# Optimization experiments

Measured on AMD Instinct MI355X. Metric: run time of the kernel, lower is better.

Reference implementation:

```python
import jax, jax.numpy as jnp
import numpy as np

# dims matching init_kwargs
B = 4096
NFIELD = 20
NFEAT = 100000
SQL_NEMB = 16
DATA_NEMB = 16
HID = 512
K = 16          # num_experts
C = 2           # select_experts (top-k)
OUT = 1
CARD = NFIELD + NFEAT + 1  # sql embedding rows
GATE_IN = NFIELD * SQL_NEMB   # 320
EXP_IN = NFIELD * DATA_NEMB   # 320
EPS = 1e-10


def _xavier(key, shape):
    fan_in, fan_out = shape[-2], shape[-1]
    a = np.sqrt(6.0 / (fan_in + fan_out)).astype(np.float32)
    return jax.random.uniform(key, shape, jnp.float32, -a, a)


def setup_inputs() -> dict:
    key = jax.random.key(0)
    ks = jax.random.split(key, 12)
    x = jax.random.randint(ks[0], (B, NFIELD), 0, NFEAT, dtype=jnp.int64)
    sql = jax.random.randint(ks[1], (B, NFIELD), 0, CARD, dtype=jnp.int64)
    return {
        "x": x,
        "sql": sql,
        "sql_emb_w": _xavier(ks[2], (CARD, SQL_NEMB)),
        "inp_emb_w": _xavier(ks[3], (NFEAT, DATA_NEMB)),
        # gate network: Linear(GATE_IN->HID) + relu + Linear(HID->K) + softmax
        "gw1": _xavier(ks[4], (GATE_IN, HID)),
        "gb1": jnp.zeros((HID,), jnp.float32),
        "gw2": _xavier(ks[5], (HID, K)),
        "gb2": jnp.zeros((K,), jnp.float32),
        # K expert DNNs: Linear(EXP_IN->HID) + relu + Linear(HID->OUT)
        "ew1": _xavier(ks[6], (K, EXP_IN, HID)),
        "eb1": jnp.zeros((K, HID), jnp.float32),
        "ew2": _xavier(ks[7], (K, HID, OUT)),
        "eb2": jnp.zeros((K, OUT), jnp.float32),
    }


def _cv_squared(v):
    # coefficient-of-variation squared, Shazeer-style load-balancing term
    return jnp.var(v) / (jnp.mean(v) ** 2 + EPS)


def reference(x, sql, sql_emb_w, inp_emb_w, gw1, gb1, gw2, gb2, ew1, eb1, ew2, eb2):
    b = x.shape[0]
    x_emb = inp_emb_w[x].reshape(b, -1)      # [B, NFIELD*DATA_NEMB]
    sql_emb = sql_emb_w[sql].reshape(b, -1)  # [B, NFIELD*SQL_NEMB]

    # gate network -> softmax scores over K experts
    h = jax.nn.relu(sql_emb @ gw1 + gb1)
    gate_scores = jax.nn.softmax(h @ gw2 + gb2, axis=-1)  # [B, K]

    # top-C sparse gating: keep top-C scores, renormalize, zero the rest
    top_v, top_i = jax.lax.top_k(gate_scores, C)
    top_v = top_v / jnp.sum(top_v, axis=-1, keepdims=True)
    gates = jnp.zeros((b, K), gate_scores.dtype).at[jnp.arange(b)[:, None], top_i].set(top_v)

    # expert MLPs (batched over expert dim; zero gates nullify unselected experts)
    eh = jax.nn.relu(jnp.einsum('bi,kih->bkh', x_emb, ew1) + eb1)   # [B, K, HID]
    eo = jnp.einsum('bkh,kho->bko', eh, ew2) + eb2                   # [B, K, OUT]
    y = jnp.sum(gates[:, :, None] * eo, axis=1).squeeze(-1)          # [B]

    importance = jnp.sum(gates, axis=0)                              # [K]
    load = jnp.sum((gates > 0).astype(gates.dtype), axis=0)         # [K]
    loss = _cv_squared(importance) + _cv_squared(load)
    return y, loss
```

## Files before the change

kernel.cpp:

```cpp
#include <hip/hip_runtime.h>

#define Bn 4096
#define NF 20
#define NEMB 16
#define HIDN 512
#define KE 16
#define GIN 320
#define NKS 10

typedef __attribute__((ext_vector_type(8))) short short8;
typedef __attribute__((ext_vector_type(4))) float f32x4;

__device__ __forceinline__ unsigned short f2bf(float f) {
  unsigned int u = __builtin_bit_cast(unsigned int, f);
  u += 0x7fff + ((u >> 16) & 1);
  return (unsigned short)(u >> 16);
}
__device__ __forceinline__ float bf2f(unsigned short h) {
  unsigned int u = ((unsigned int)h) << 16;
  return __builtin_bit_cast(float, u);
}

__device__ __forceinline__ void gload_lds16(const unsigned short* g, void* l) {
  __builtin_amdgcn_global_load_lds(
      (const __attribute__((address_space(1))) unsigned int*)g,
      (__attribute__((address_space(3))) unsigned int*)l, 16, 0, 0);
}

__device__ __forceinline__ void vwait(int n) {
  if (n >= 5) asm volatile("s_waitcnt vmcnt(5)" ::: "memory");
  else        asm volatile("s_waitcnt vmcnt(0)" ::: "memory");
  __builtin_amdgcn_sched_barrier(0);
}

__global__ __launch_bounds__(256) void prep_kernel(
    const int* __restrict__ sql, const float* __restrict__ semb,
    const float* __restrict__ gw1, const float* __restrict__ ew1,
    unsigned short* __restrict__ SH, unsigned short* __restrict__ SL,
    unsigned short* __restrict__ GWF, unsigned short* __restrict__ EWF,
    float* __restrict__ y, int* __restrict__ cnt) {
  long long t = (long long)blockIdx.x * 256 + threadIdx.x;
  if (t < 81920) {
    int row = (int)(t / NF), f = (int)(t % NF);
    int idx = sql[row * NF + f];
    const float4* s = (const float4*)(semb + (size_t)idx * NEMB);
    float4 v[4] = {s[0], s[1], s[2], s[3]};
    const float* sf = (const float*)v;
    short8 h0, h1, l0, l1;
#pragma unroll
    for (int i = 0; i < 8; i++) {
      float a = sf[i];
      unsigned short hb = f2bf(a);
      h0[i] = (short)hb; l0[i] = (short)f2bf(a - bf2f(hb));
      a = sf[8 + i];
      hb = f2bf(a);
      h1[i] = (short)hb; l1[i] = (short)f2bf(a - bf2f(hb));
    }
    size_t o = (size_t)row * GIN + f * NEMB;
    *(short8*)(SH + o) = h0; *(short8*)(SH + o + 8) = h1;
    *(short8*)(SL + o) = l0; *(short8*)(SL + o + 8) = l1;
    return;
  }
  t -= 81920;
  if (t < 40960) {
    int s = (int)(t / 20480), r = (int)(t % 20480);
    int ks = r / 2048, r2 = r % 2048, nt = r2 / 64, l = r2 % 64;
    int k0 = ks * 32 + (l >> 4) * 8, n = nt * 16 + (l & 15);
    short8 o;
#pragma unroll
    for (int j = 0; j < 8; j++) {
      float w = gw1[(size_t)(k0 + j) * HIDN + n];
      unsigned short hb = f2bf(w);
      o[j] = (s == 0) ? (short)hb : (short)f2bf(w - bf2f(hb));
    }
    *(short8*)(GWF + ((((size_t)s * NKS + ks) * 32 + nt) * 64 + l) * 8) = o;
    return;
  }
  t -= 40960;
  if (t < 327680) {
    int e = (int)(t / 20480), r = (int)(t % 20480);
    int ks = r / 2048, r2 = r % 2048, nt = r2 / 64, l = r2 % 64;
    int k0 = ks * 32 + (l >> 4) * 8, n = nt * 16 + (l & 15);
    const float* W = ew1 + (size_t)e * GIN * HIDN;
    short8 o;
#pragma unroll
    for (int j = 0; j < 8; j++) o[j] = (short)f2bf(W[(size_t)(k0 + j) * HIDN + n]);
    *(short8*)(EWF + ((((size_t)e * NKS + ks) * 32 + nt) * 64 + l) * 8) = o;
    return;
  }
  t -= 327680;
  if (t < Bn + 1) y[t] = 0.f;
  else if (t < Bn + 1 + KE) cnt[t - (Bn + 1)] = 0;
}

__global__ __launch_bounds__(256, 2) void gate_kernel(
    const unsigned short* __restrict__ SH, const unsigned short* __restrict__ SL,
    const unsigned short* __restrict__ GWF, const float* __restrict__ gb1,
    const float* __restrict__ gw2, float* __restrict__ glp) {
  __shared__ __align__(16) unsigned short ring[3][10240];
  __shared__ float hs[64][68];
  const int tid = threadIdx.x, lane = tid & 63, wv = tid >> 6;
  const int band = blockIdx.x * 64, cb = blockIdx.y;
  const int ntg = cb * 4 + wv;

  short8 bh[NKS], bl[NKS];
#pragma unroll
  for (int ks = 0; ks < NKS; ks++) {
    bh[ks] = *(const short8*)(GWF + ((size_t)(ks * 32 + ntg)) * 512 + lane * 8);
    bl[ks] = *(const short8*)(GWF + ((size_t)((NKS + ks) * 32 + ntg)) * 512 + lane * 8);
  }
  const int cl = wv * 16 + (lane & 15);
  const float b1v = gb1[cb * 64 + cl];
  __builtin_amdgcn_sched_barrier(0);

#define GSTG(pi, slot)                                                        \
  {                                                                           \
    _Pragma("unroll") for (int i = 0; i < 5; i++) {                           \
      int c = wv * 5 + i;                                                     \
      int hl = c >= 10, kss = c - hl * 10;                                    \
      const unsigned short* s_ = (hl ? SL : SH) +                             \
          (size_t)(band + (pi) * 16 + (lane & 15)) * GIN + kss * 32 +         \
          (lane >> 4) * 8;                                                    \
      gload_lds16(s_, &ring[slot][c * 512 + lane * 8]);                       \
    }                                                                         \
  }

  GSTG(0, 0) GSTG(1, 1)
  __builtin_amdgcn_sched_barrier(0);

#pragma unroll
  for (int p = 0; p < 4; p++) {
    vwait(p < 3 ? 5 : 0);
    __builtin_amdgcn_s_barrier();
    __builtin_amdgcn_sched_barrier(0);
    if (p + 2 < 4) GSTG(p + 2, (p + 2) % 3)
    __builtin_amdgcn_sched_barrier(0);
    const unsigned short* rb = ring[p % 3];
    f32x4 acc = {};
#pragma unroll
    for (int ks = 0; ks < NKS; ks++) {
      short8 ah = *(const short8*)&rb[ks * 512 + lane * 8];
      short8 al = *(const short8*)&rb[(NKS + ks) * 512 + lane * 8];
      acc = __builtin_amdgcn_mfma_f32_16x16x32_bf16(ah, bh[ks], acc, 0, 0, 0);
      acc = __builtin_amdgcn_mfma_f32_16x16x32_bf16(al, bh[ks], acc, 0, 0, 0);
      acc = __builtin_amdgcn_mfma_f32_16x16x32_bf16(ah, bl[ks], acc, 0, 0, 0);
    }
#pragma unroll
    for (int j = 0; j < 4; j++)
      hs[p * 16 + (lane >> 4) * 4 + j][cl] = fmaxf(acc[j] + b1v, 0.f);
  }
  __syncthreads();

  float (*g2s)[16] = (float(*)[16])&ring[0][0];
  ((float4*)g2s)[tid] = ((const float4*)(gw2 + (size_t)cb * 64 * KE))[tid];
  __syncthreads();
#pragma unroll
  for (int it = 0; it < 4; it++) {
    int row = it * 16 + (tid >> 4), q = tid & 15;
    float s = 0.f;
#pragma unroll 8
    for (int c = 0; c < 64; c++) s = fmaf(hs[row][c], g2s[c][q], s);
    glp[((size_t)cb * Bn + band + row) * KE + q] = s;
  }
#undef GSTG
}

__global__ __launch_bounds__(256) void gate2_kernel(
    const float* __restrict__ glp, const float* __restrict__ gb2,
    int* __restrict__ cnt, int* __restrict__ list, float* __restrict__ wlist) {
  __shared__ int lcnt[KE];
  __shared__ int gbase[KE];
  const int tid = threadIdx.x;
  const int row = blockIdx.x * 256 + tid;
  if (tid < KE) lcnt[tid] = 0;
  __syncthreads();
  float lg[KE];
  {
    const float4* c = (const float4*)gb2;
#pragma unroll
    for (int u = 0; u < 4; u++) {
      float4 s = c[u];
      lg[u * 4 + 0] = s.x; lg[u * 4 + 1] = s.y;
      lg[u * 4 + 2] = s.z; lg[u * 4 + 3] = s.w;
    }
#pragma unroll
    for (int sl = 0; sl < 8; sl++) {
      const float4* a = (const float4*)(glp + ((size_t)sl * Bn + row) * KE);
#pragma unroll
      for (int u = 0; u < 4; u++) {
        float4 v = a[u];
        lg[u * 4 + 0] += v.x; lg[u * 4 + 1] += v.y;
        lg[u * 4 + 2] += v.z; lg[u * 4 + 3] += v.w;
      }
    }
  }
  float m = lg[0];
#pragma unroll
  for (int q = 1; q < KE; q++) m = fmaxf(m, lg[q]);
  float e[KE];
#pragma unroll
  for (int q = 0; q < KE; q++) e[q] = expf(lg[q] - m);
  int i1 = 0; float v1 = e[0];
#pragma unroll
  for (int q = 1; q < KE; q++) if (e[q] > v1) { v1 = e[q]; i1 = q; }
  int i2 = (i1 == 0) ? 1 : 0; float v2 = e[i2];
#pragma unroll
  for (int q = 0; q < KE; q++)
    if (q != i1 && e[q] > v2) { v2 = e[q]; i2 = q; }
  int o1 = atomicAdd(&lcnt[i1], 1);
  int o2 = atomicAdd(&lcnt[i2], 1);
  __syncthreads();
  if (tid < KE) gbase[tid] = atomicAdd(&cnt[tid], lcnt[tid]);
  __syncthreads();
  float den = v1 + v2;
  int s1 = gbase[i1] + o1;
  list[i1 * Bn + s1] = row; wlist[i1 * Bn + s1] = v1 / den;
  int s2 = gbase[i2] + o2;
  list[i2 * Bn + s2] = row; wlist[i2 * Bn + s2] = v2 / den;
}

__global__ __launch_bounds__(256) void packloss_kernel(
    const int* __restrict__ x, const float* __restrict__ demb,
    const int* __restrict__ cnt, const int* __restrict__ list,
    const float* __restrict__ wlist, unsigned short* __restrict__ XEP,
    float* __restrict__ out) {
  __shared__ float simp[KE][KE];
  __shared__ float fimp[KE];
  const int tid = threadIdx.x;
  const int jb = blockIdx.x, k = blockIdx.y;
  if (jb == 64) {
    if (k != 0) return;
    const int kk = tid >> 4, g = tid & 15;
    const int n = cnt[kk];
    float s = 0.f;
    for (int j = g; j < n; j += 16) s += wlist[kk * Bn + j];
    simp[kk][g] = s;
    __syncthreads();
    if (tid < KE) {
      float t = 0.f;
      for (int q = 0; q < KE; q++) t += simp[tid][q];
      fimp[tid] = t;
    }
    __syncthreads();
    if (tid == 0) {
      double mi = 0.0, ml = 0.0;
      for (int q = 0; q < KE; q++) { mi += fimp[q]; ml += (double)cnt[q]; }
      mi /= KE; ml /= KE;
      double vi = 0.0, vl = 0.0;
      for (int q = 0; q < KE; q++) {
        double di = fimp[q] - mi; vi += di * di;
        double dl = (double)cnt[q] - ml; vl += dl * dl;
      }
      vi /= KE; vl /= KE;
      out[Bn] = (float)(vi / (mi * mi + 1e-10) + vl / (ml * ml + 1e-10));
    }
    return;
  }
  const int n = cnt[k];
  if (jb * 64 >= n) return;
  unsigned short* reg = XEP + (size_t)k * 1310720;
#pragma unroll
  for (int it = 0; it < 5; it++) {
    int tt = it * 256 + tid;
    int i = jb * 64 + tt / NF, f = tt % NF;
    if (i < n) {
      int rid = list[k * Bn + i];
      int idx = x[rid * NF + f];
      const float4* s = (const float4*)(demb + (size_t)idx * NEMB);
      float4 v[4] = {s[0], s[1], s[2], s[3]};
      const float* sf = (const float*)v;
      short8 o0, o1;
#pragma unroll
      for (int e = 0; e < 8; e++) {
        o0[e] = (short)f2bf(sf[e]);
        o1[e] = (short)f2bf(sf[8 + e]);
      }
      int panel = i >> 5, mt = (i >> 4) & 1, lr = i & 15;
      int ks = f >> 1, ko0 = (f & 1) * 2;
      unsigned short* d =
          reg + (size_t)panel * 10240 + ks * 1024 + mt * 512 + ko0 * 128 + lr * 8;
      *(short8*)d = o0;
      *(short8*)(d + 128) = o1;
    }
  }
}

__global__ __launch_bounds__(256, 2) void expert_kernel(
    const unsigned short* __restrict__ XEP, const unsigned short* __restrict__ EWF,
    const float* __restrict__ eb1, const float* __restrict__ ew2,
    const float* __restrict__ eb2, const int* __restrict__ cnt,
    const int* __restrict__ list, const float* __restrict__ wlist,
    float* __restrict__ y) {
  __shared__ __align__(16) unsigned short ring[3][10240];
  __shared__ float pb[16][4][32];
  const int tid = threadIdx.x, lane = tid & 63, wv = tid >> 6;
  const int cb = blockIdx.x, k = blockIdx.y, qz = blockIdx.z;
  const int n = cnt[k];
  const int np = (n + 31) >> 5;
  const int npb = (np > qz) ? ((np - qz + 7) >> 3) : 0;
  if (npb == 0) return;
  const unsigned short* XEPk = XEP + (size_t)k * 1310720;
  const int kBn = k * Bn;

  float b1v[2], w2v[2];
#pragma unroll
  for (int nt = 0; nt < 2; nt++) {
    int colg = cb * 128 + (wv * 2 + nt) * 16 + (lane & 15);
    b1v[nt] = eb1[(size_t)k * HIDN + colg];
    w2v[nt] = ew2[(size_t)k * HIDN + colg];
  }
  short8 bb[2][NKS];
#pragma unroll
  for (int nt = 0; nt < 2; nt++)
#pragma unroll
    for (int ks = 0; ks < NKS; ks++)
      bb[nt][ks] = *(const short8*)(
          EWF + ((size_t)((k * NKS + ks) * 32 + cb * 8 + wv * 2 + nt)) * 512 +
          lane * 8);
  __builtin_amdgcn_sched_barrier(0);

#define ESTG(pi, slot)                                                        \
  {                                                                           \
    _Pragma("unroll") for (int i = 0; i < 5; i++) {                           \
      int c = wv * 5 + i;                                                     \
      gload_lds16(XEPk + (size_t)(pi) * 10240 + c * 512 + lane * 8,           \
                  &ring[slot][c * 512 + lane * 8]);                           \
    }                                                                         \
  }

  ESTG(qz, 0)
  if (npb > 1) ESTG(qz + 8, 1)
  __builtin_amdgcn_sched_barrier(0);

  for (int p = 0; p < npb; p++) {
    vwait((p + 1 < npb) ? 5 : 0);
    __builtin_amdgcn_s_barrier();
    __builtin_amdgcn_sched_barrier(0);
    if (p + 2 < npb) ESTG(qz + 8 * (p + 2), (p + 2) % 3)
    __builtin_amdgcn_sched_barrier(0);
    const unsigned short* rb = ring[p % 3];
    f32x4 acc[2][2] = {};
#pragma unroll
    for (int ks = 0; ks < NKS; ks++) {
      short8 a0 = *(const short8*)&rb[ks * 1024 + lane * 8];
      short8 a1 = *(const short8*)&rb[ks * 1024 + 512 + lane * 8];
      acc[0][0] = __builtin_amdgcn_mfma_f32_16x16x32_bf16(a0, bb[0][ks], acc[0][0], 0, 0, 0);
      acc[0][1] = __builtin_amdgcn_mfma_f32_16x16x32_bf16(a0, bb[1][ks], acc[0][1], 0, 0, 0);
      acc[1][0] = __builtin_amdgcn_mfma_f32_16x16x32_bf16(a1, bb[0][ks], acc[1][0], 0, 0, 0);
      acc[1][1] = __builtin_amdgcn_mfma_f32_16x16x32_bf16(a1, bb[1][ks], acc[1][1], 0, 0, 0);
    }
    float part[2][4];
#pragma unroll
    for (int mt = 0; mt < 2; mt++)
#pragma unroll
      for (int j = 0; j < 4; j++)
        part[mt][j] = fmaxf(acc[mt][0][j] + b1v[0], 0.f) * w2v[0] +
                      fmaxf(acc[mt][1][j] + b1v[1], 0.f) * w2v[1];
#pragma unroll
    for (int off = 8; off >= 1; off >>= 1)
#pragma unroll
      for (int mt = 0; mt < 2; mt++)
#pragma unroll
        for (int j = 0; j < 4; j++)
          part[mt][j] += __shfl_xor(part[mt][j], off);
    if ((lane & 15) == 0) {
#pragma unroll
      for (int mt = 0; mt < 2; mt++)
#pragma unroll
        for (int j = 0; j < 4; j++)
          pb[p][wv][mt * 16 + (lane >> 4) * 4 + j] = part[mt][j];
    }
  }
  __syncthreads();

  const float e2 = (cb == 0) ? eb2[k] : 0.f;
  for (int t = tid; t < npb * 32; t += 256) {
    int pp = t >> 5, r = t & 31;
    int i = (qz + 8 * pp) * 32 + r;
    if (i < n) {
      float v = pb[pp][0][r] + pb[pp][1][r] + pb[pp][2][r] + pb[pp][3][r];
      atomicAdd(&y[list[kBn + i]], wlist[kBn + i] * (v + e2));
    }
  }
#undef ESTG
}

extern "C" void kernel_launch(void* const* d_in, const int* in_sizes, int n_in,
                              void* d_out, int out_size, void* d_ws, size_t ws_size,
                              hipStream_t stream) {
  const int* x      = (const int*)d_in[0];
  const int* sql    = (const int*)d_in[1];
  const float* semb = (const float*)d_in[2];
  const float* demb = (const float*)d_in[3];
  const float* gw1  = (const float*)d_in[4];
  const float* gb1  = (const float*)d_in[5];
  const float* gw2  = (const float*)d_in[6];
  const float* gb2  = (const float*)d_in[7];
  const float* ew1  = (const float*)d_in[8];
  const float* eb1  = (const float*)d_in[9];
  const float* ew2  = (const float*)d_in[10];
  const float* eb2  = (const float*)d_in[11];
  float* y = (float*)d_out;

  char* ws = (char*)d_ws;
  int* cnt            = (int*)(ws);
  int* list           = (int*)(ws + 4096);
  float* wlist        = (float*)(ws + 266240);
  float* glp          = (float*)(ws + 528384);
  unsigned short* SH  = (unsigned short*)(ws + 5246976);
  unsigned short* SL  = (unsigned short*)(ws + 7868416);
  unsigned short* GWF = (unsigned short*)(ws + 10489856);
  unsigned short* EWF = (unsigned short*)(ws + 11145216);
  unsigned short* XEP = (unsigned short*)(ws + 16777216);

  prep_kernel<<<1777, 256, 0, stream>>>(sql, semb, gw1, ew1,
                                        SH, SL, GWF, EWF, y, cnt);
  gate_kernel<<<dim3(64, 8), 256, 0, stream>>>(SH, SL, GWF, gb1, gw2, glp);
  gate2_kernel<<<Bn / 256, 256, 0, stream>>>(glp, gb2, cnt, list, wlist);
  packloss_kernel<<<dim3(65, 16), 256, 0, stream>>>(x, demb, cnt, list, wlist,
                                                    XEP, y);
  expert_kernel<<<dim3(4, 16, 8), 256, 0, stream>>>(XEP, EWF, eb1, ew2, eb2,
                                                    cnt, list, wlist, y);
}
```

Baseline: 72.02 us.

## Remap block indices for XCD locality and split gate2 reduction across waves

Flattens the gate, packloss and expert grids to 1D and remaps block ids. Blocks that share an expert (k) or a batch band then land on the same XCD, which improves per-XCD L2 reuse of weights and packed inputs. gate2 now uses 64-row blocks where four waves each sum two of the eight partial-logit slices into shared memory. Wave 0 then does the softmax, top-2 selection and list scatter, so the kernel runs on more blocks. The gate2 barriers now sit inside a wave-uniform branch, which is fragile but matched.

```diff
diff --git a/kernel.cpp b/kernel.cpp
--- a/kernel.cpp
+++ b/kernel.cpp
@@ -100,7 +100,10 @@
   __shared__ __align__(16) unsigned short ring[3][10240];
   __shared__ float hs[64][68];
   const int tid = threadIdx.x, lane = tid & 63, wv = tid >> 6;
-  const int band = blockIdx.x * 64, cb = blockIdx.y;
+  const int bid = blockIdx.x;
+  const int xcd = bid & 7, r_ = bid >> 3;
+  const int cb = r_ & 7;
+  const int band = (8 * xcd + (r_ >> 3)) * 64;
   const int ntg = cb * 4 + wv;
 
   short8 bh[NKS], bl[NKS];
@@ -168,55 +171,62 @@
 __global__ __launch_bounds__(256) void gate2_kernel(
     const float* __restrict__ glp, const float* __restrict__ gb2,
     int* __restrict__ cnt, int* __restrict__ list, float* __restrict__ wlist) {
+  __shared__ float part[4][64][KE];
   __shared__ int lcnt[KE];
   __shared__ int gbase[KE];
   const int tid = threadIdx.x;
-  const int row = blockIdx.x * 256 + tid;
+  const int r = tid & 63, g = tid >> 6;
+  const int row = blockIdx.x * 64 + r;
   if (tid < KE) lcnt[tid] = 0;
+  float lg[KE];
+#pragma unroll
+  for (int q = 0; q < KE; q++) lg[q] = 0.f;
+#pragma unroll
+  for (int s2 = 0; s2 < 2; s2++) {
+    const float4* a = (const float4*)(glp + ((size_t)(2 * g + s2) * Bn + row) * KE);
+#pragma unroll
+    for (int u = 0; u < 4; u++) {
+      float4 v = a[u];
+      lg[u * 4 + 0] += v.x; lg[u * 4 + 1] += v.y;
+      lg[u * 4 + 2] += v.z; lg[u * 4 + 3] += v.w;
+    }
+  }
+#pragma unroll
+  for (int q = 0; q < KE; q++) part[g][r][q] = lg[q];
   __syncthreads();
-  float lg[KE];
-  {
-    const float4* c = (const float4*)gb2;
-#pragma unroll
-    for (int u = 0; u < 4; u++) {
-      float4 s = c[u];
-      lg[u * 4 + 0] = s.x; lg[u * 4 + 1] = s.y;
-      lg[u * 4 + 2] = s.z; lg[u * 4 + 3] = s.w;
-    }
-#pragma unroll
-    for (int sl = 0; sl < 8; sl++) {
-      const float4* a = (const float4*)(glp + ((size_t)sl * Bn + row) * KE);
-#pragma unroll
-      for (int u = 0; u < 4; u++) {
-        float4 v = a[u];
-        lg[u * 4 + 0] += v.x; lg[u * 4 + 1] += v.y;
-        lg[u * 4 + 2] += v.z; lg[u * 4 + 3] += v.w;
-      }
-    }
-  }
-  float m = lg[0];
-#pragma unroll
-  for (int q = 1; q < KE; q++) m = fmaxf(m, lg[q]);
-  float e[KE];
-#pragma unroll
-  for (int q = 0; q < KE; q++) e[q] = expf(lg[q] - m);
-  int i1 = 0; float v1 = e[0];
-#pragma unroll
-  for (int q = 1; q < KE; q++) if (e[q] > v1) { v1 = e[q]; i1 = q; }
-  int i2 = (i1 == 0) ? 1 : 0; float v2 = e[i2];
-#pragma unroll
-  for (int q = 0; q < KE; q++)
-    if (q != i1 && e[q] > v2) { v2 = e[q]; i2 = q; }
-  int o1 = atomicAdd(&lcnt[i1], 1);
-  int o2 = atomicAdd(&lcnt[i2], 1);
-  __syncthreads();
-  if (tid < KE) gbase[tid] = atomicAdd(&cnt[tid], lcnt[tid]);
-  __syncthreads();
-  float den = v1 + v2;
-  int s1 = gbase[i1] + o1;
-  list[i1 * Bn + s1] = row; wlist[i1 * Bn + s1] = v1 / den;
-  int s2 = gbase[i2] + o2;
-  list[i2 * Bn + s2] = row; wlist[i2 * Bn + s2] = v2 / den;
+  if (tid < 64) {
+#pragma unroll
+    for (int q = 0; q < KE; q++)
+      lg[q] = part[0][tid][q] + part[1][tid][q] + part[2][tid][q] +
+              part[3][tid][q] + gb2[q];
+    float m = lg[0];
+#pragma unroll
+    for (int q = 1; q < KE; q++) m = fmaxf(m, lg[q]);
+    float e[KE];
+#pragma unroll
+    for (int q = 0; q < KE; q++) e[q] = expf(lg[q] - m);
+    int i1 = 0; float v1 = e[0];
+#pragma unroll
+    for (int q = 1; q < KE; q++) if (e[q] > v1) { v1 = e[q]; i1 = q; }
+    int i2 = (i1 == 0) ? 1 : 0; float v2 = e[i2];
+#pragma unroll
+    for (int q = 0; q < KE; q++)
+      if (q != i1 && e[q] > v2) { v2 = e[q]; i2 = q; }
+    int rowg = blockIdx.x * 64 + tid;
+    int o1 = atomicAdd(&lcnt[i1], 1);
+    int o2 = atomicAdd(&lcnt[i2], 1);
+    __syncthreads();
+    if (tid < KE) gbase[tid] = atomicAdd(&cnt[tid], lcnt[tid]);
+    __syncthreads();
+    float den = v1 + v2;
+    int s1 = gbase[i1] + o1;
+    list[i1 * Bn + s1] = rowg; wlist[i1 * Bn + s1] = v1 / den;
+    int s2 = gbase[i2] + o2;
+    list[i2 * Bn + s2] = rowg; wlist[i2 * Bn + s2] = v2 / den;
+  } else {
+    __syncthreads();
+    __syncthreads();
+  }
 }
 
 __global__ __launch_bounds__(256) void packloss_kernel(
@@ -227,7 +237,9 @@
   __shared__ float simp[KE][KE];
   __shared__ float fimp[KE];
   const int tid = threadIdx.x;
-  const int jb = blockIdx.x, k = blockIdx.y;
+  const int bid = blockIdx.x;
+  const int xcd = bid & 7, r_ = bid >> 3;
+  const int k = xcd + 8 * (r_ & 1), jb = r_ >> 1;
   if (jb == 64) {
     if (k != 0) return;
     const int kk = tid >> 4, g = tid & 15;
@@ -294,7 +306,10 @@
   __shared__ __align__(16) unsigned short ring[3][10240];
   __shared__ float pb[16][4][32];
   const int tid = threadIdx.x, lane = tid & 63, wv = tid >> 6;
-  const int cb = blockIdx.x, k = blockIdx.y, qz = blockIdx.z;
+  const int bid = blockIdx.x;
+  const int xcd = bid & 7, r_ = bid >> 3;
+  const int k = xcd + 8 * (r_ & 1);
+  const int cb = (r_ >> 1) & 3, qz = r_ >> 3;
   const int n = cnt[k];
   const int np = (n + 31) >> 5;
   const int npb = (np > qz) ? ((np - qz + 7) >> 3) : 0;
@@ -415,10 +430,9 @@
 
   prep_kernel<<<1777, 256, 0, stream>>>(sql, semb, gw1, ew1,
                                         SH, SL, GWF, EWF, y, cnt);
-  gate_kernel<<<dim3(64, 8), 256, 0, stream>>>(SH, SL, GWF, gb1, gw2, glp);
-  gate2_kernel<<<Bn / 256, 256, 0, stream>>>(glp, gb2, cnt, list, wlist);
-  packloss_kernel<<<dim3(65, 16), 256, 0, stream>>>(x, demb, cnt, list, wlist,
-                                                    XEP, y);
-  expert_kernel<<<dim3(4, 16, 8), 256, 0, stream>>>(XEP, EWF, eb1, ew2, eb2,
-                                                    cnt, list, wlist, y);
-}
+  gate_kernel<<<512, 256, 0, stream>>>(SH, SL, GWF, gb1, gw2, glp);
+  gate2_kernel<<<64, 256, 0, stream>>>(glp, gb2, cnt, list, wlist);
+  packloss_kernel<<<1040, 256, 0, stream>>>(x, demb, cnt, list, wlist, XEP, y);
+  expert_kernel<<<512, 256, 0, stream>>>(XEP, EWF, eb1, ew2, eb2,
+                                         cnt, list, wlist, y);
+}
```

New measurement: 72.81 us. About the same (+1.1%).
